# Kernel optimization log

Measured on AMD Instinct MI355X. Metric: run time of the kernel, lower is better.

The kernel has to match this reference:

```python
import jax, jax.numpy as jnp
import numpy as np

BLOCK_M = 64          # Triton BLOCK_M assumed from first autotune config
SPEAKER, SCENE, STAGE = 1, 2, 3
NUM_HEADS, HEAD_SIZE = 12, 64


def setup_inputs() -> dict:
    key = jax.random.key(0)
    ks = jax.random.split(key, 6)
    B, T, E = 4, 1024, 768
    H, D = NUM_HEADS, HEAD_SIZE
    x = jax.random.normal(ks[0], (B, T, E), jnp.float32)
    idx = jax.random.randint(ks[1], (B, T), 0, 32000)
    struct_embed = jax.random.normal(ks[2], (4, E), jnp.float32) * 0.02
    w_qkv = jax.random.normal(ks[3], (3 * H * D, E), jnp.float32) * 0.02
    w_out = jax.random.normal(ks[4], (E, H * D), jnp.float32) * 0.02
    b_out = jnp.zeros((E,), jnp.float32)
    return {"x": x, "idx": idx, "struct_embed": struct_embed,
            "w_qkv": w_qkv, "w_out": w_out, "b_out": b_out}


def _attention(q, k, v):
    # q,k,v: [B,H,T,D]. Faithful to the Triton kernel (eval mode):
    # q/k rounded to bf16, fp32 dot, logit clamp [-30,30], exp clamp 1e5,
    # +1e-10 denom, output rounded to bf16. Query rows with
    # (row % BLOCK_M) % 3 == 0 are zeroed by the kernel's load mask.
    T, D = q.shape[2], q.shape[3]
    keep = ((jnp.arange(T) % BLOCK_M) % 3 != 0).astype(q.dtype)
    qb = q.astype(jnp.bfloat16).astype(jnp.float32) * keep[None, None, :, None]
    kb = k.astype(jnp.bfloat16).astype(jnp.float32)
    scale = 1.0 / np.sqrt(D).astype(np.float32)
    scores = jnp.einsum('bhmd,bhnd->bhmn', qb, kb) * scale
    scores = jnp.clip(scores, -30.0, 30.0)
    m = jnp.max(scores, axis=-1, keepdims=True)
    p = jnp.minimum(jnp.exp(scores - m), 1e5)
    acc = jnp.einsum('bhmn,bhnd->bhmd', p, v)
    out = acc / (jnp.sum(p, axis=-1, keepdims=True) + 1e-10)
    return out.astype(jnp.bfloat16).astype(jnp.float32)


def reference(x, idx, struct_embed, w_qkv, w_out, b_out):
    B, T, E = x.shape
    H, D = NUM_HEADS, HEAD_SIZE
    # structure embedding addition (struct_dropout is identity in eval)
    struct_ids = ((idx == SPEAKER) * 1 + (idx == SCENE) * 2
                  + (idx == STAGE) * 3)
    x = x + struct_embed[struct_ids]
    # fused QKV projection (no bias)
    qkv = x @ w_qkv.T                              # [B,T,3HD]
    q, k, v = jnp.split(qkv, 3, axis=-1)
    q = q.reshape(B, T, H, D).transpose(0, 2, 1, 3)
    k = k.reshape(B, T, H, D).transpose(0, 2, 1, 3)
    v = v.reshape(B, T, H, D).transpose(0, 2, 1, 3)
    attn = _attention(q, k, v)                     # [B,H,T,D]
    attn = attn.transpose(0, 2, 1, 3).reshape(B, T, H * D)
    return attn @ w_out.T + b_out
```

## Files before the change

kernel.cpp:

```cpp
#include <hip/hip_runtime.h>
#include <hip/hip_bf16.h>

typedef __attribute__((ext_vector_type(8))) short bf16x8;
typedef __attribute__((ext_vector_type(4))) float f32x4;

#define MFMA16(a, b, c) __builtin_amdgcn_mfma_f32_16x16x32_bf16(a, b, c, 0, 0, 0)
#define VMCNT4() asm volatile("s_waitcnt vmcnt(4)" ::: "memory")
#define VMCNT0() asm volatile("s_waitcnt vmcnt(0)" ::: "memory")

__device__ __forceinline__ unsigned short f2bf(float f) {
  unsigned u = __float_as_uint(f);
  u += 0x7fff + ((u >> 16) & 1);
  return (unsigned short)(u >> 16);
}
__device__ __forceinline__ float bf2f(unsigned short s) {
  return __uint_as_float(((unsigned)s) << 16);
}
__device__ __forceinline__ void gload16(const unsigned short* g, unsigned short* l) {
  __builtin_amdgcn_global_load_lds((const __attribute__((address_space(1))) void*)g,
                                   (__attribute__((address_space(3))) void*)l, 16, 0, 0);
}
__device__ __forceinline__ int xcd_swz(int lin, int nwg) {
  int cpx = nwg >> 3;
  return (lin & 7) * cpx + (lin >> 3);
}

__global__ __launch_bounds__(256) void prep_all(const float* __restrict__ x,
                                                const int* __restrict__ idx,
                                                const float* __restrict__ se,
                                                const float* __restrict__ wqkv,
                                                const float* __restrict__ wout,
                                                unsigned short* __restrict__ xb,
                                                unsigned short* __restrict__ wqkvb,
                                                unsigned short* __restrict__ woutb) {
  int bid = blockIdx.x;
  int tid = threadIdx.x;
  if (bid < 3072) {
    int i = bid * 256 + tid;
    int row = i / 192, c4 = i % 192;
    int id = idx[row];
    int sid = (id == 1) ? 1 : (id == 2) ? 2 : (id == 3) ? 3 : 0;
    float4 v = ((const float4*)x)[i];
    float4 s = ((const float4*)se)[sid * 192 + c4];
    ushort4 o;
    o.x = f2bf(v.x + s.x); o.y = f2bf(v.y + s.y);
    o.z = f2bf(v.z + s.z); o.w = f2bf(v.w + s.w);
    *(ushort4*)(xb + (size_t)i * 4) = o;
  } else if (bid < 3072 + 1728) {
    int i = (bid - 3072) * 256 + tid;
    float4 v = ((const float4*)wqkv)[i];
    ushort4 u;
    u.x = f2bf(v.x); u.y = f2bf(v.y); u.z = f2bf(v.z); u.w = f2bf(v.w);
    ((ushort4*)wqkvb)[i] = u;
  } else {
    int i = (bid - 4800) * 256 + tid;
    float4 v = ((const float4*)wout)[i];
    ushort4 u;
    u.x = f2bf(v.x); u.y = f2bf(v.y); u.z = f2bf(v.z); u.w = f2bf(v.w);
    ((ushort4*)woutb)[i] = u;
  }
}

__global__ __launch_bounds__(256) void gemm_qkv(const unsigned short* __restrict__ A,
                                                const unsigned short* __restrict__ B,
                                                unsigned short* __restrict__ Cout,
                                                unsigned short* __restrict__ vT,
                                                int N, int K) {
  __shared__ unsigned short As[2][4096];
  __shared__ unsigned short Bs[2][4096];
  int tid = threadIdx.x;
  int lane = tid & 63, wid = tid >> 6;
  int l15 = lane & 15, lhi = lane >> 4;
  int wr = wid >> 1, wc = wid & 1;
  int gy = gridDim.y;
  int lin = blockIdx.x + gridDim.x * blockIdx.y;
  int swz = xcd_swz(lin, gridDim.x * gy);
  long tm = (long)(swz / gy) * 128;
  long tn = (long)(swz % gy) * 128;
  f32x4 acc[4][4];
  const f32x4 z4 = {0.f, 0.f, 0.f, 0.f};
  for (int i = 0; i < 4; ++i)
    for (int j = 0; j < 4; ++j) acc[i][j] = z4;

  int wbase = tid & ~63;
  int row0 = tid >> 2;
  int kc = (tid & 3) * 8;
  const unsigned short* Ar0 = &A[(tm + row0) * (long)K + kc];
  const unsigned short* Ar1 = &A[(tm + 64 + row0) * (long)K + kc];
  const unsigned short* Br0 = &B[(tn + row0) * (long)K + kc];
  const unsigned short* Br1 = &B[(tn + 64 + row0) * (long)K + kc];

  auto stage = [&](int b, int k0) {
    gload16(Ar0 + k0, &As[b][wbase * 8]);
    gload16(Ar1 + k0, &As[b][2048 + wbase * 8]);
    gload16(Br0 + k0, &Bs[b][wbase * 8]);
    gload16(Br1 + k0, &Bs[b][2048 + wbase * 8]);
  };

  stage(0, 0);
  __syncthreads();
  int buf = 0;
  for (int k0 = 0; k0 < K; k0 += 32) {
    if (k0 + 32 < K) stage(buf ^ 1, k0 + 32);
    bf16x8 af[4], bfr[4];
#pragma unroll
    for (int mi = 0; mi < 4; ++mi)
      af[mi] = *(const bf16x8*)&As[buf][(wr * 64 + mi * 16 + l15) * 32 + lhi * 8];
#pragma unroll
    for (int nj = 0; nj < 4; ++nj)
      bfr[nj] = *(const bf16x8*)&Bs[buf][(wc * 64 + nj * 16 + l15) * 32 + lhi * 8];
#pragma unroll
    for (int mi = 0; mi < 4; ++mi)
#pragma unroll
      for (int nj = 0; nj < 4; ++nj)
        acc[mi][nj] = MFMA16(af[mi], bfr[nj], acc[mi][nj]);
    __syncthreads();
    buf ^= 1;
  }

  if (tn >= 1536) {
    int b = (int)(tm >> 10);
    int hbase = (int)((tn - 1536) >> 6) + wc;
    int tmw = (int)(tm & 1023) + wr * 64;
#pragma unroll
    for (int nj = 0; nj < 4; ++nj) {
      int dd = nj * 16 + l15;
      size_t vbase = ((size_t)(b * 12 + hbase)) * 65536 + (size_t)dd * 1024;
#pragma unroll
      for (int mi = 0; mi < 4; ++mi) {
        ushort4 o;
        o.x = f2bf(acc[mi][nj][0]); o.y = f2bf(acc[mi][nj][1]);
        o.z = f2bf(acc[mi][nj][2]); o.w = f2bf(acc[mi][nj][3]);
        *(ushort4*)&vT[vbase + tmw + (mi >> 1) * 32 + lhi * 8 + (mi & 1) * 4] = o;
      }
    }
    return;
  }

#pragma unroll
  for (int mi = 0; mi < 4; ++mi) {
    long row = tm + wr * 64 + mi * 16 + lhi * 4;
#pragma unroll
    for (int nj = 0; nj < 4; ++nj) {
      long col = tn + wc * 64 + nj * 16 + l15;
#pragma unroll
      for (int r = 0; r < 4; ++r)
        Cout[(row + r) * (long)N + col] = f2bf(acc[mi][nj][r]);
    }
  }
}

__global__ __launch_bounds__(256) void gemm_out(const unsigned short* __restrict__ A,
                                                const unsigned short* __restrict__ B,
                                                float* __restrict__ Cout,
                                                const float* __restrict__ bias,
                                                int N, int K) {
  __shared__ unsigned short As[2][64 * 32];
  __shared__ unsigned short Bs[2][64 * 32];
  int tid = threadIdx.x;
  int lane = tid & 63, w = tid >> 6;
  int l15 = lane & 15, lhi = lane >> 4;
  int gy = gridDim.y;
  int lin = blockIdx.x + gridDim.x * blockIdx.y;
  int swz = xcd_swz(lin, gridDim.x * gy);
  long tm = (long)(swz / gy) * 64;
  long tn = (long)(swz % gy) * 64;
  f32x4 acc[4];
  const f32x4 z4 = {0.f, 0.f, 0.f, 0.f};
#pragma unroll
  for (int n = 0; n < 4; ++n) acc[n] = z4;

  int wbase8 = (tid & ~63) * 8;
  int row0 = tid >> 2;
  int kc = (tid & 3) * 8;
  const unsigned short* Ar = &A[(tm + row0) * (long)K + kc];
  const unsigned short* Br = &B[(tn + row0) * (long)K + kc];

  auto stage = [&](int b, int k0) {
    gload16(Ar + k0, &As[b][wbase8]);
    gload16(Br + k0, &Bs[b][wbase8]);
  };

  stage(0, 0);
  __syncthreads();
  int buf = 0;
  for (int k0 = 0; k0 < K; k0 += 32) {
    if (k0 + 32 < K) stage(buf ^ 1, k0 + 32);
    bf16x8 af = *(const bf16x8*)&As[buf][(w * 16 + l15) * 32 + lhi * 8];
    bf16x8 bfr[4];
#pragma unroll
    for (int n = 0; n < 4; ++n)
      bfr[n] = *(const bf16x8*)&Bs[buf][(n * 16 + l15) * 32 + lhi * 8];
#pragma unroll
    for (int n = 0; n < 4; ++n)
      acc[n] = MFMA16(af, bfr[n], acc[n]);
    __syncthreads();
    buf ^= 1;
  }

  long row = tm + w * 16 + lhi * 4;
#pragma unroll
  for (int n = 0; n < 4; ++n) {
    long col = tn + n * 16 + l15;
    float bv = bias[col];
#pragma unroll
    for (int r = 0; r < 4; ++r)
      Cout[(row + r) * (long)N + col] = acc[n][r] + bv;
  }
}

__global__ __launch_bounds__(256) void attn_fwd(const unsigned short* __restrict__ qkv,
                                                const unsigned short* __restrict__ vT,
                                                unsigned short* __restrict__ attnb) {
  __shared__ unsigned short Ks[3][4096];
  __shared__ unsigned short Vs[3][4096];
  int tid = threadIdx.x;
  int lane = tid & 63, w = tid >> 6;
  int l15 = lane & 15, lhi = lane >> 4;
  int sw = l15 & 7;
  int lin = blockIdx.x + gridDim.x * blockIdx.y;
  int swz = xcd_swz(lin, 768);
  int qt = swz & 15, bh = swz >> 4;
  int b = bh / 12, h = bh % 12;

  int qrl = w * 16 + l15;
  bf16x8 qf0 = {0, 0, 0, 0, 0, 0, 0, 0}, qf1 = {0, 0, 0, 0, 0, 0, 0, 0};
  if (qrl % 3 != 0) {
    const unsigned short* qp =
        &qkv[(size_t)(b * 1024 + qt * 64 + qrl) * 2304 + h * 64 + lhi * 8];
    qf0 = *(const bf16x8*)qp;
    qf1 = *(const bf16x8*)(qp + 32);
  }

  int r8 = lane >> 3;
  int cK = ((lane & 7) ^ r8) << 3;
  int wbase = (tid & ~63) * 8;
  const unsigned short* kg = qkv + (size_t)(b * 1024) * 2304 + 768 + h * 64 + cK;
  const unsigned short* vg = vT + (size_t)bh * 65536 + cK;

  auto stage = [&](int bufi, int t) {
    size_t k0 = (size_t)t * 64;
#pragma unroll
    for (int p = 0; p < 2; ++p) {
      int row = p * 32 + w * 8 + r8;
      gload16(kg + (k0 + row) * 2304, &Ks[bufi][p * 2048 + wbase]);
      gload16(vg + (size_t)row * 1024 + k0, &Vs[bufi][p * 2048 + wbase]);
    }
  };

  stage(0, 0);
  stage(1, 1);

  const f32x4 z4 = {0.f, 0.f, 0.f, 0.f};
  f32x4 acc[4];
#pragma unroll
  for (int dg = 0; dg < 4; ++dg) acc[dg] = z4;
  f32x4 accd = z4;
  const short one_bf = (short)0x3F80;
  const bf16x8 ONES = {one_bf, one_bf, one_bf, one_bf, one_bf, one_bf, one_bf, one_bf};

  int bc = 0, bp = 2;
  for (int t = 0; t < 16; ++t) {
    if (t < 15) VMCNT4(); else VMCNT0();
    __builtin_amdgcn_s_barrier();
    if (t + 2 < 16) stage(bp, t + 2);
    const unsigned short* ks = Ks[bc];
    const unsigned short* vs = Vs[bc];

    bf16x8 kf[4][2];
#pragma unroll
    for (int g = 0; g < 4; ++g) {
      const unsigned short* kr = &ks[(g * 16 + l15) * 64];
      kf[g][0] = *(const bf16x8*)&kr[(lhi ^ sw) << 3];
      kf[g][1] = *(const bf16x8*)&kr[((lhi + 4) ^ sw) << 3];
    }
    bf16x8 vfr[4][2];
#pragma unroll
    for (int dg = 0; dg < 4; ++dg) {
      const unsigned short* vr = &vs[(dg * 16 + l15) * 64];
#pragma unroll
      for (int kh = 0; kh < 2; ++kh)
        vfr[dg][kh] = *(const bf16x8*)&vr[((kh * 4 + lhi) ^ sw) << 3];
    }

    bf16x8 paf[2];
#pragma unroll
    for (int g = 0; g < 4; ++g) {
      f32x4 sg = MFMA16(kf[g][0], qf0, z4);
      sg = MFMA16(kf[g][1], qf1, sg);
#pragma unroll
      for (int r = 0; r < 4; ++r) {
        float pv = exp2f(sg[r] * 0.18033688011f);
        paf[g >> 1][(g & 1) * 4 + r] = (short)f2bf(pv);
      }
    }

    __builtin_amdgcn_s_setprio(1);
    accd = MFMA16(paf[0], ONES, accd);
    accd = MFMA16(paf[1], ONES, accd);
#pragma unroll
    for (int dg = 0; dg < 4; ++dg)
#pragma unroll
      for (int kh = 0; kh < 2; ++kh)
        acc[dg] = MFMA16(paf[kh], vfr[dg][kh], acc[dg]);
    __builtin_amdgcn_s_setprio(0);
    bc = (bc == 2) ? 0 : bc + 1;
    bp = (bp == 2) ? 0 : bp + 1;
  }

#pragma unroll
  for (int r = 0; r < 4; ++r) {
    float inv = 1.f / (accd[r] + 1e-10f);
    int orow = qt * 64 + w * 16 + lhi * 4 + r;
    size_t obase = (size_t)(b * 1024 + orow) * 768 + h * 64;
#pragma unroll
    for (int dg = 0; dg < 4; ++dg)
      attnb[obase + dg * 16 + l15] = f2bf(acc[dg][r] * inv);
  }
}

extern "C" void kernel_launch(void* const* d_in, const int* in_sizes, int n_in,
                              void* d_out, int out_size, void* d_ws, size_t ws_size,
                              hipStream_t stream) {
  (void)in_sizes; (void)n_in; (void)out_size; (void)ws_size;
  const float* x    = (const float*)d_in[0];
  const int*   idx  = (const int*)d_in[1];
  const float* se   = (const float*)d_in[2];
  const float* wqkv = (const float*)d_in[3];
  const float* wout = (const float*)d_in[4];
  const float* bout = (const float*)d_in[5];
  float* out = (float*)d_out;

  char* ws = (char*)d_ws;
  unsigned short* xb    = (unsigned short*)(ws);
  unsigned short* wqkvb = (unsigned short*)(ws + 6291456);
  unsigned short* woutb = (unsigned short*)(ws + 9830400);
  unsigned short* qkvb  = (unsigned short*)(ws + 11010048);
  unsigned short* vT    = (unsigned short*)(ws + 29884416);
  unsigned short* attnb = (unsigned short*)(ws + 36175872);

  prep_all<<<5376, 256, 0, stream>>>(x, idx, se, wqkv, wout, xb, wqkvb, woutb);
  gemm_qkv<<<dim3(32, 18), 256, 0, stream>>>(xb, wqkvb, qkvb, vT, 2304, 768);
  attn_fwd<<<dim3(16, 48), 256, 0, stream>>>(qkvb, vT, attnb);
  gemm_out<<<dim3(64, 12), 256, 0, stream>>>(attnb, woutb, out, bout, 768, 768);
}
```

Baseline: 82.54 us.

## Halve attention block to two waves, each handling two 16-row query tiles

The attention kernel now runs with 128 threads (2 waves) instead of 256. Each wave processes two 16-row query sub-tiles and reuses each K/V fragment read from LDS for both, so LDS reads per useful MFMA are halved. Each thread issues twice as many global-to-LDS loads per stage, and the wait count is raised to match. Softmax probabilities are also packed into 32-bit words before the bitcast. The trade-off is higher register pressure per wave and fewer waves per block to hide latency.

```diff
diff --git a/kernel.cpp b/kernel.cpp
--- a/kernel.cpp
+++ b/kernel.cpp
@@ -5,16 +5,13 @@
 typedef __attribute__((ext_vector_type(4))) float f32x4;
 
 #define MFMA16(a, b, c) __builtin_amdgcn_mfma_f32_16x16x32_bf16(a, b, c, 0, 0, 0)
-#define VMCNT4() asm volatile("s_waitcnt vmcnt(4)" ::: "memory")
+#define VMCNT8() asm volatile("s_waitcnt vmcnt(8)" ::: "memory")
 #define VMCNT0() asm volatile("s_waitcnt vmcnt(0)" ::: "memory")
 
 __device__ __forceinline__ unsigned short f2bf(float f) {
   unsigned u = __float_as_uint(f);
   u += 0x7fff + ((u >> 16) & 1);
   return (unsigned short)(u >> 16);
-}
-__device__ __forceinline__ float bf2f(unsigned short s) {
-  return __uint_as_float(((unsigned)s) << 16);
 }
 __device__ __forceinline__ void gload16(const unsigned short* g, unsigned short* l) {
   __builtin_amdgcn_global_load_lds((const __attribute__((address_space(1))) void*)g,
@@ -209,7 +206,7 @@
   }
 }
 
-__global__ __launch_bounds__(256) void attn_fwd(const unsigned short* __restrict__ qkv,
+__global__ __launch_bounds__(128) void attn_fwd(const unsigned short* __restrict__ qkv,
                                                 const unsigned short* __restrict__ vT,
                                                 unsigned short* __restrict__ attnb) {
   __shared__ unsigned short Ks[3][4096];
@@ -223,28 +220,33 @@
   int qt = swz & 15, bh = swz >> 4;
   int b = bh / 12, h = bh % 12;
 
-  int qrl = w * 16 + l15;
-  bf16x8 qf0 = {0, 0, 0, 0, 0, 0, 0, 0}, qf1 = {0, 0, 0, 0, 0, 0, 0, 0};
-  if (qrl % 3 != 0) {
-    const unsigned short* qp =
-        &qkv[(size_t)(b * 1024 + qt * 64 + qrl) * 2304 + h * 64 + lhi * 8];
-    qf0 = *(const bf16x8*)qp;
-    qf1 = *(const bf16x8*)(qp + 32);
+  bf16x8 qf[2][2];
+#pragma unroll
+  for (int u = 0; u < 2; ++u) {
+    qf[u][0] = bf16x8{0, 0, 0, 0, 0, 0, 0, 0};
+    qf[u][1] = bf16x8{0, 0, 0, 0, 0, 0, 0, 0};
+    int qrl = w * 32 + u * 16 + l15;
+    if (qrl % 3 != 0) {
+      const unsigned short* qp =
+          &qkv[(size_t)(b * 1024 + qt * 64 + qrl) * 2304 + h * 64 + lhi * 8];
+      qf[u][0] = *(const bf16x8*)qp;
+      qf[u][1] = *(const bf16x8*)(qp + 32);
+    }
   }
 
   int r8 = lane >> 3;
   int cK = ((lane & 7) ^ r8) << 3;
-  int wbase = (tid & ~63) * 8;
+  int wb512 = w * 512;
   const unsigned short* kg = qkv + (size_t)(b * 1024) * 2304 + 768 + h * 64 + cK;
   const unsigned short* vg = vT + (size_t)bh * 65536 + cK;
 
   auto stage = [&](int bufi, int t) {
     size_t k0 = (size_t)t * 64;
 #pragma unroll
-    for (int p = 0; p < 2; ++p) {
-      int row = p * 32 + w * 8 + r8;
-      gload16(kg + (k0 + row) * 2304, &Ks[bufi][p * 2048 + wbase]);
-      gload16(vg + (size_t)row * 1024 + k0, &Vs[bufi][p * 2048 + wbase]);
+    for (int p = 0; p < 4; ++p) {
+      int row = p * 16 + w * 8 + r8;
+      gload16(kg + (k0 + row) * 2304, &Ks[bufi][p * 1024 + wb512]);
+      gload16(vg + (size_t)row * 1024 + k0, &Vs[bufi][p * 1024 + wb512]);
     }
   };
 
@@ -252,16 +254,18 @@
   stage(1, 1);
 
   const f32x4 z4 = {0.f, 0.f, 0.f, 0.f};
-  f32x4 acc[4];
-#pragma unroll
-  for (int dg = 0; dg < 4; ++dg) acc[dg] = z4;
-  f32x4 accd = z4;
+  f32x4 acc[2][4];
+#pragma unroll
+  for (int u = 0; u < 2; ++u)
+#pragma unroll
+    for (int dg = 0; dg < 4; ++dg) acc[u][dg] = z4;
+  f32x4 accd[2] = {z4, z4};
   const short one_bf = (short)0x3F80;
   const bf16x8 ONES = {one_bf, one_bf, one_bf, one_bf, one_bf, one_bf, one_bf, one_bf};
 
   int bc = 0, bp = 2;
   for (int t = 0; t < 16; ++t) {
-    if (t < 15) VMCNT4(); else VMCNT0();
+    if (t < 15) VMCNT8(); else VMCNT0();
     __builtin_amdgcn_s_barrier();
     if (t + 2 < 16) stage(bp, t + 2);
     const unsigned short* ks = Ks[bc];
@@ -283,39 +287,59 @@
         vfr[dg][kh] = *(const bf16x8*)&vr[((kh * 4 + lhi) ^ sw) << 3];
     }
 
-    bf16x8 paf[2];
+    int4 pw[2][2];
 #pragma unroll
     for (int g = 0; g < 4; ++g) {
-      f32x4 sg = MFMA16(kf[g][0], qf0, z4);
-      sg = MFMA16(kf[g][1], qf1, sg);
-#pragma unroll
-      for (int r = 0; r < 4; ++r) {
-        float pv = exp2f(sg[r] * 0.18033688011f);
-        paf[g >> 1][(g & 1) * 4 + r] = (short)f2bf(pv);
+#pragma unroll
+      for (int u = 0; u < 2; ++u) {
+        f32x4 sg = MFMA16(kf[g][0], qf[u][0], z4);
+        sg = MFMA16(kf[g][1], qf[u][1], sg);
+        float p0 = exp2f(sg[0] * 0.18033688011f);
+        float p1 = exp2f(sg[1] * 0.18033688011f);
+        float p2 = exp2f(sg[2] * 0.18033688011f);
+        float p3 = exp2f(sg[3] * 0.18033688011f);
+        int w01 = (int)((unsigned)f2bf(p0) | ((unsigned)f2bf(p1) << 16));
+        int w23 = (int)((unsigned)f2bf(p2) | ((unsigned)f2bf(p3) << 16));
+        if ((g & 1) == 0) { pw[u][g >> 1].x = w01; pw[u][g >> 1].y = w23; }
+        else              { pw[u][g >> 1].z = w01; pw[u][g >> 1].w = w23; }
       }
     }
+    bf16x8 paf[2][2];
+#pragma unroll
+    for (int u = 0; u < 2; ++u)
+#pragma unroll
+      for (int kh = 0; kh < 2; ++kh)
+        paf[u][kh] = __builtin_bit_cast(bf16x8, pw[u][kh]);
 
     __builtin_amdgcn_s_setprio(1);
-    accd = MFMA16(paf[0], ONES, accd);
-    accd = MFMA16(paf[1], ONES, accd);
+#pragma unroll
+    for (int u = 0; u < 2; ++u) {
+      accd[u] = MFMA16(paf[u][0], ONES, accd[u]);
+      accd[u] = MFMA16(paf[u][1], ONES, accd[u]);
+    }
 #pragma unroll
     for (int dg = 0; dg < 4; ++dg)
 #pragma unroll
       for (int kh = 0; kh < 2; ++kh)
-        acc[dg] = MFMA16(paf[kh], vfr[dg][kh], acc[dg]);
+#pragma unroll
+        for (int u = 0; u < 2; ++u)
+          acc[u][dg] = MFMA16(paf[u][kh], vfr[dg][kh], acc[u][dg]);
     __builtin_amdgcn_s_setprio(0);
     bc = (bc == 2) ? 0 : bc + 1;
     bp = (bp == 2) ? 0 : bp + 1;
   }
 
 #pragma unroll
-  for (int r = 0; r < 4; ++r) {
-    float inv = 1.f / (accd[r] + 1e-10f);
-    int orow = qt * 64 + w * 16 + lhi * 4 + r;
-    size_t obase = (size_t)(b * 1024 + orow) * 768 + h * 64;
-#pragma unroll
-    for (int dg = 0; dg < 4; ++dg)
-      attnb[obase + dg * 16 + l15] = f2bf(acc[dg][r] * inv);
+  for (int u = 0; u < 2; ++u) {
+#pragma unroll
+    for (int r = 0; r < 4; ++r) {
+      float inv = 1.f / (accd[u][r] + 1e-10f);
+      int orow = qt * 64 + w * 32 + u * 16 + lhi * 4 + r;
+      size_t obase = (size_t)(b * 1024 + orow) * 768 + h * 64;
+#pragma unroll
+      for (int dg = 0; dg < 4; ++dg)
+        attnb[obase + dg * 16 + l15] = f2bf(acc[u][dg][r] * inv);
+    }
   }
 }
 
@@ -341,6 +365,6 @@
 
   prep_all<<<5376, 256, 0, stream>>>(x, idx, se, wqkv, wout, xb, wqkvb, woutb);
   gemm_qkv<<<dim3(32, 18), 256, 0, stream>>>(xb, wqkvb, qkvb, vT, 2304, 768);
-  attn_fwd<<<dim3(16, 48), 256, 0, stream>>>(qkvb, vT, attnb);
+  attn_fwd<<<dim3(16, 48), 128, 0, stream>>>(qkvb, vT, attnb);
   gemm_out<<<dim3(64, 12), 256, 0, stream>>>(attnb, woutb, out, bout, 768, 768);
 }
```

Result: slower. 90.92 us (+10.1%).
